# Performance work log

Hardware: AMD Instinct MI355X
Metric: run time of the kernel (lower is better)

Reference implementation:

```python
import jax, jax.numpy as jnp
import numpy as np

NEG_INF = -9e15
ALPHA = 0.2  # LeakyReLU negative slope

N = 8192
D_IN = 512
D_OUT = 256


def setup_inputs() -> dict:
    key = jax.random.key(0)
    k1, k2, k3, k4, k5 = jax.random.split(key, 5)
    features = jax.random.normal(k1, (N, D_IN), dtype=jnp.float32)
    adjacency_matrix = jax.random.randint(k2, (N, N), 0, 2, dtype=jnp.int32)
    # learned params (torch Linear stores [out, in]; we use [in, out] layout)
    s_phi = 1.0 / np.sqrt(D_IN)
    W_phi = jax.random.uniform(k3, (D_IN, D_OUT), jnp.float32, -s_phi, s_phi)
    s_v = 1.0 / np.sqrt(D_OUT)
    w_mu = jax.random.uniform(k4, (D_OUT,), jnp.float32, -s_v, s_v)
    w_xi = jax.random.uniform(k5, (D_OUT,), jnp.float32, -s_v, s_v)
    return {"features": features, "adjacency_matrix": adjacency_matrix,
            "W_phi": W_phi, "w_mu": w_mu, "w_xi": w_xi}


def reference(features, adjacency_matrix, W_phi, w_mu, w_xi):
    h = features @ W_phi                                   # [N, d_out]
    mu = h @ w_mu                                          # [N]
    xi = h @ w_xi                                          # [N]
    e = mu[:, None] + xi[None, :]                          # [N, N] additive scores
    e = jnp.where(e >= 0, e, ALPHA * e)                    # LeakyReLU
    e = jnp.where(adjacency_matrix > 0, e, NEG_INF)        # mask non-edges
    a = jax.nn.softmax(e, axis=1)                          # row softmax (dropout p=0)
    out = a @ h                                            # weighted aggregation
    return jax.nn.elu(out)
```

## Files before the change

kernel.cpp:

```cpp
#include <hip/hip_runtime.h>
#include <cstdint>
#include <cstddef>


#define NN 8192
#define DIN 512
#define DOUT 256

typedef __attribute__((ext_vector_type(8))) short short8;
typedef __attribute__((ext_vector_type(4))) float floatx4;

using uint_as1 = __attribute__((address_space(1))) unsigned int;
using uint_as3 = __attribute__((address_space(3))) unsigned int;

__device__ __forceinline__ void gld_lds16(const void* g, void* l) {
  __builtin_amdgcn_global_load_lds((const uint_as1*)g, (uint_as3*)l, 16, 0, 0);
}

__device__ __forceinline__ unsigned short f2b(float f) {
  unsigned u = __float_as_uint(f);
  u += 0x7fffu + ((u >> 16) & 1u);
  return (unsigned short)(u >> 16);
}
__device__ __forceinline__ float b2f(short s) {
  return __uint_as_float(((unsigned)(unsigned short)s) << 16);
}

__global__ void k_cvt_features(const float* __restrict__ f, unsigned short* __restrict__ fb) {
  int tid = blockIdx.x * 256 + threadIdx.x;
  float4 v = ((const float4*)f)[tid];
  ushort4 o = {f2b(v.x), f2b(v.y), f2b(v.z), f2b(v.w)};
  *(ushort4*)&fb[tid * 4] = o;
}

__global__ void k_prep_wt(const float* __restrict__ w, unsigned short* __restrict__ wt) {
  int tid = blockIdx.x * 256 + threadIdx.x;
  int n = tid >> 9, k = tid & 511;
  wt[n * 512 + k] = f2b(w[k * 256 + n]);
}

__global__ void k_prep_p(const float* __restrict__ w, const float* __restrict__ wmu,
                         const float* __restrict__ wxi, float* __restrict__ pmu,
                         float* __restrict__ pxi) {
  int tid = blockIdx.x * 256 + threadIdx.x;
  int k = tid >> 2, seg = tid & 3;
  float sm = 0.f, sx = 0.f;
  int base = k * 256 + seg * 64;
#pragma unroll
  for (int c = 0; c < 64; c += 4) {
    float4 wv = *(const float4*)&w[base + c];
    float4 mv = *(const float4*)&wmu[seg * 64 + c];
    float4 xv = *(const float4*)&wxi[seg * 64 + c];
    sm += wv.x * mv.x + wv.y * mv.y + wv.z * mv.z + wv.w * mv.w;
    sx += wv.x * xv.x + wv.y * xv.y + wv.z * xv.z + wv.w * xv.w;
  }
  sm += __shfl_xor(sm, 1); sm += __shfl_xor(sm, 2);
  sx += __shfl_xor(sx, 1); sx += __shfl_xor(sx, 2);
  if (seg == 0) { pmu[k] = sm; pxi[k] = sx; }
}

__global__ void k_mu_xi(const unsigned short* __restrict__ fb, const float* __restrict__ pmu,
                        const float* __restrict__ pxi, float* __restrict__ mu,
                        float* __restrict__ xi) {
  int w = threadIdx.x >> 6, l = threadIdx.x & 63;
  int i = blockIdx.x * 4 + w;
  short8 fv = *(const short8*)&fb[i * 512 + l * 8];
  float m = 0.f, x = 0.f;
#pragma unroll
  for (int c = 0; c < 8; ++c) {
    float fvf = b2f(fv[c]);
    m = fmaf(fvf, pmu[l * 8 + c], m);
    x = fmaf(fvf, pxi[l * 8 + c], x);
  }
#pragma unroll
  for (int off = 32; off > 0; off >>= 1) {
    m += __shfl_xor(m, off);
    x += __shfl_xor(x, off);
  }
  if (l == 0) { mu[i] = m; xi[i] = x; }
}

__global__ __launch_bounds__(256, 2) void k_gemm1(const unsigned short* __restrict__ fb,
                                                  const unsigned short* __restrict__ wt,
                                                  unsigned short* __restrict__ ht) {
  __shared__ __align__(16) unsigned short As[64 * 64];
  __shared__ __align__(16) unsigned short Bs[128 * 64];
  int t = threadIdx.x, w = t >> 6, l = t & 63;
  int bm = blockIdx.x >> 1, bn = blockIdx.x & 1;
  int m0 = bm * 64, n0 = bn * 128;
  int lr = l >> 3, lg = l & 7, g = lg ^ lr;
  int kg = l >> 4, ln = l & 15;
  floatx4 zero = {0.f, 0.f, 0.f, 0.f};
  floatx4 acc[4][2];
#pragma unroll
  for (int mf = 0; mf < 4; ++mf)
#pragma unroll
    for (int nf = 0; nf < 2; ++nf) acc[mf][nf] = zero;

  for (int it = 0; it < 8; ++it) {
    int k0 = it * 64;
#pragma unroll
    for (int q = 0; q < 2; ++q) {
      int row = w * 16 + q * 8 + lr;
      const void* gp = fb + (size_t)(m0 + row) * 512 + k0 + g * 8;
      int lb = __builtin_amdgcn_readfirstlane((w * 16 + q * 8) * 64);
      gld_lds16(gp, &As[lb]);
    }
#pragma unroll
    for (int q = 0; q < 4; ++q) {
      int row = w * 32 + q * 8 + lr;
      const void* gp = wt + (size_t)(n0 + row) * 512 + k0 + g * 8;
      int lb = __builtin_amdgcn_readfirstlane((w * 32 + q * 8) * 64);
      gld_lds16(gp, &Bs[lb]);
    }
    __syncthreads();
#pragma unroll
    for (int ks = 0; ks < 2; ++ks) {
      int gg = ks * 4 + kg;
      int swz = (gg ^ (ln & 7)) * 8;
      short8 bfr[2];
#pragma unroll
      for (int nf = 0; nf < 2; ++nf)
        bfr[nf] = *(const short8*)&Bs[(w * 32 + nf * 16 + ln) * 64 + swz];
#pragma unroll
      for (int mf = 0; mf < 4; ++mf) {
        short8 afr = *(const short8*)&As[(mf * 16 + ln) * 64 + swz];
#pragma unroll
        for (int nf = 0; nf < 2; ++nf)
          acc[mf][nf] = __builtin_amdgcn_mfma_f32_16x16x32_bf16(afr, bfr[nf], acc[mf][nf], 0, 0, 0);
      }
    }
    __syncthreads();
  }
#pragma unroll
  for (int mf = 0; mf < 4; ++mf)
#pragma unroll
    for (int nf = 0; nf < 2; ++nf) {
      int ng = n0 + w * 32 + nf * 16 + ln;
      int mg = m0 + mf * 16 + kg * 4;
      ushort4 o = {f2b(acc[mf][nf][0]), f2b(acc[mf][nf][1]),
                   f2b(acc[mf][nf][2]), f2b(acc[mf][nf][3])};
      *(ushort4*)&ht[(size_t)ng * 8192 + mg] = o;
    }
}

__global__ __launch_bounds__(256, 2) void k_attn(const int* __restrict__ adj,
                                                 const unsigned short* __restrict__ ht,
                                                 const float* __restrict__ mu,
                                                 const float* __restrict__ xi,
                                                 float* __restrict__ out) {
  __shared__ __align__(16) unsigned short Bt[256 * 64];
  __shared__ __align__(16) unsigned short Wl[16 * 72];
  __shared__ __align__(16) float xis[8192];
  __shared__ float zinv[16];

  int t = threadIdx.x, w = t >> 6, l = t & 63;
  int i0 = blockIdx.x * 16;
  int rowi = t >> 4, col4 = (t & 15) * 4;
  int lr = l >> 3, lg = l & 7, g = lg ^ lr;
  int kg = l >> 4, ln = l & 15;

  float mu_t = mu[i0 + rowi];
#pragma unroll
  for (int c = 0; c < 8; ++c) {
    int idx = c * 1024 + t * 4;
    *(float4*)&xis[idx] = *(const float4*)&xi[idx];
  }
  floatx4 zero = {0.f, 0.f, 0.f, 0.f};
  floatx4 acc[4];
#pragma unroll
  for (int nf = 0; nf < 4; ++nf) acc[nf] = zero;
  float zsum = 0.f;
  const int* adjrow = adj + (size_t)(i0 + rowi) * 8192 + col4;
  __syncthreads();

  for (int it = 0; it < 128; ++it) {
    int j0 = it * 64;
    int4 a4 = *(const int4*)(adjrow + j0);
    float4 xv = *(const float4*)&xis[j0 + col4];
    float s0 = mu_t + xv.x, s1 = mu_t + xv.y, s2 = mu_t + xv.z, s3 = mu_t + xv.w;
    s0 = fmaxf(s0, 0.2f * s0); s1 = fmaxf(s1, 0.2f * s1);
    s2 = fmaxf(s2, 0.2f * s2); s3 = fmaxf(s3, 0.2f * s3);
    float e0 = __builtin_amdgcn_exp2f(s0 * 1.44269504f);
    float e1 = __builtin_amdgcn_exp2f(s1 * 1.44269504f);
    float e2 = __builtin_amdgcn_exp2f(s2 * 1.44269504f);
    float e3 = __builtin_amdgcn_exp2f(s3 * 1.44269504f);
    float w0 = (a4.x != 0) ? e0 : 0.f;
    float w1 = (a4.y != 0) ? e1 : 0.f;
    float w2 = (a4.z != 0) ? e2 : 0.f;
    float w3 = (a4.w != 0) ? e3 : 0.f;
    zsum += (w0 + w1) + (w2 + w3);
    ushort4 wp = {f2b(w0), f2b(w1), f2b(w2), f2b(w3)};
    *(ushort4*)&Wl[rowi * 72 + col4] = wp;
#pragma unroll
    for (int q = 0; q < 8; ++q) {
      int n = w * 64 + q * 8 + lr;
      const void* gp = ht + (size_t)n * 8192 + j0 + g * 8;
      int lb = __builtin_amdgcn_readfirstlane((w * 64 + q * 8) * 64);
      gld_lds16(gp, &Bt[lb]);
    }
    __syncthreads();
#pragma unroll
    for (int ks = 0; ks < 2; ++ks) {
      int gg = ks * 4 + kg;
      short8 afr = *(const short8*)&Wl[ln * 72 + gg * 8];
#pragma unroll
      for (int nf = 0; nf < 4; ++nf) {
        int n = w * 64 + nf * 16 + ln;
        short8 bfr = *(const short8*)&Bt[n * 64 + ((gg ^ (ln & 7)) * 8)];
        acc[nf] = __builtin_amdgcn_mfma_f32_16x16x32_bf16(afr, bfr, acc[nf], 0, 0, 0);
      }
    }
    __syncthreads();
  }

  float* zb = xis;
  zb[t] = zsum;
  __syncthreads();
  if (t < 16) {
    float s = 0.f;
#pragma unroll
    for (int q = 0; q < 16; ++q) s += zb[t * 16 + q];
    zinv[t] = 1.0f / s;
  }
  __syncthreads();

#pragma unroll
  for (int nf = 0; nf < 4; ++nf) {
    int col = w * 64 + nf * 16 + ln;
#pragma unroll
    for (int r = 0; r < 4; ++r) {
      int row = kg * 4 + r;
      float v = acc[nf][r] * zinv[row];
      v = (v > 0.f) ? v : (__builtin_amdgcn_exp2f(v * 1.44269504f) - 1.f);
      out[(size_t)(i0 + row) * 256 + col] = v;
    }
  }
}

extern "C" void kernel_launch(void* const* d_in, const int* in_sizes, int n_in,
                              void* d_out, int out_size, void* d_ws, size_t ws_size,
                              hipStream_t stream) {
  const float* features = (const float*)d_in[0];
  const int* adjm = (const int*)d_in[1];
  const float* W_phi = (const float*)d_in[2];
  const float* w_mu = (const float*)d_in[3];
  const float* w_xi = (const float*)d_in[4];
  float* out = (float*)d_out;

  char* ws = (char*)d_ws;
  unsigned short* fb  = (unsigned short*)(ws + 0);
  unsigned short* ht  = (unsigned short*)(ws + 8388608);
  unsigned short* wt  = (unsigned short*)(ws + 12582912);
  float* pmu = (float*)(ws + 12845056);
  float* pxi = (float*)(ws + 12847104);
  float* muv = (float*)(ws + 12849152);
  float* xiv = (float*)(ws + 12881920);

  k_cvt_features<<<4096, 256, 0, stream>>>(features, fb);
  k_prep_wt<<<512, 256, 0, stream>>>(W_phi, wt);
  k_prep_p<<<8, 256, 0, stream>>>(W_phi, w_mu, w_xi, pmu, pxi);
  k_mu_xi<<<2048, 256, 0, stream>>>(fb, pmu, pxi, muv, xiv);
  k_gemm1<<<256, 256, 0, stream>>>(fb, wt, ht);
  k_attn<<<512, 256, 0, stream>>>(adjm, ht, muv, xiv, out);
}
```

Before: 505.9 us.

## Split attention aggregation across column chunks with atomic partial sums

The attention kernel now gives each block 64 rows and a quarter of the columns (split-K). The B operand (ht) is read straight from global memory into registers instead of being staged through LDS, and adjacency loads are prefetched one iteration ahead. Partial numerators and softmax denominators are accumulated with float atomics into a zeroed workspace, and a separate final kernel normalizes and applies ELU. This removes the per-iteration barriers and the LDS staging, and each block reads ht once for 64 rows instead of 16. The cost is the atomic traffic, two extra launches, and summation order that is no longer deterministic. It also holds 16 accumulator tiles per thread, which raises register pressure.

```diff
diff --git a/kernel.cpp b/kernel.cpp
--- a/kernel.cpp
+++ b/kernel.cpp
@@ -144,98 +144,119 @@
     }
 }
 
-__global__ __launch_bounds__(256, 2) void k_attn(const int* __restrict__ adj,
-                                                 const unsigned short* __restrict__ ht,
-                                                 const float* __restrict__ mu,
-                                                 const float* __restrict__ xi,
-                                                 float* __restrict__ out) {
-  __shared__ __align__(16) unsigned short Bt[256 * 64];
-  __shared__ __align__(16) unsigned short Wl[16 * 72];
-  __shared__ __align__(16) float xis[8192];
-  __shared__ float zinv[16];
-
+__global__ void k_zero(float* __restrict__ num, float* __restrict__ zbuf) {
+  int b = blockIdx.x, t = threadIdx.x;
+  if (b < 2048) {
+    float4 z4 = {0.f, 0.f, 0.f, 0.f};
+    *(float4*)&num[(b * 256 + t) * 4] = z4;
+  } else {
+    zbuf[(b - 2048) * 256 + t] = 0.f;
+  }
+}
+
+__global__ __launch_bounds__(256, 2) void k_attn3(const int* __restrict__ adj,
+                                                  const unsigned short* __restrict__ ht,
+                                                  const float* __restrict__ mu,
+                                                  const float* __restrict__ xi,
+                                                  float* __restrict__ num,
+                                                  float* __restrict__ zbuf) {
+  __shared__ __align__(16) float xic[2048];
   int t = threadIdx.x, w = t >> 6, l = t & 63;
-  int i0 = blockIdx.x * 16;
-  int rowi = t >> 4, col4 = (t & 15) * 4;
-  int lr = l >> 3, lg = l & 7, g = lg ^ lr;
-  int kg = l >> 4, ln = l & 15;
-
-  float mu_t = mu[i0 + rowi];
-#pragma unroll
-  for (int c = 0; c < 8; ++c) {
-    int idx = c * 1024 + t * 4;
-    *(float4*)&xis[idx] = *(const float4*)&xi[idx];
-  }
+  int ln = l & 15, kg = l >> 4;
+  int bi = blockIdx.x >> 2, bj = blockIdx.x & 3;
+  int i0 = bi * 64, jbase = bj * 2048;
+
+#pragma unroll
+  for (int c = 0; c < 2; ++c) {
+    int idx = t * 8 + c * 4;
+    float4 v = *(const float4*)&xi[jbase + idx];
+    v.x *= 1.44269504f; v.y *= 1.44269504f; v.z *= 1.44269504f; v.w *= 1.44269504f;
+    *(float4*)&xic[idx] = v;
+  }
+  int irow = i0 + w * 16 + ln;
+  float mu_c = mu[irow] * 1.44269504f;
+  __syncthreads();
+
   floatx4 zero = {0.f, 0.f, 0.f, 0.f};
-  floatx4 acc[4];
-#pragma unroll
-  for (int nf = 0; nf < 4; ++nf) acc[nf] = zero;
+  floatx4 acc[16];
+#pragma unroll
+  for (int nf = 0; nf < 16; ++nf) acc[nf] = zero;
+
+  const int4* ap = (const int4*)(adj + (size_t)irow * 8192 + jbase) + kg * 2;
+  int4 a0 = ap[0], a1 = ap[1], b0 = ap[8], b1 = ap[9];
+  const unsigned short* hrow = ht + (size_t)ln * 8192 + jbase + kg * 8;
   float zsum = 0.f;
-  const int* adjrow = adj + (size_t)(i0 + rowi) * 8192 + col4;
-  __syncthreads();
-
-  for (int it = 0; it < 128; ++it) {
-    int j0 = it * 64;
-    int4 a4 = *(const int4*)(adjrow + j0);
-    float4 xv = *(const float4*)&xis[j0 + col4];
-    float s0 = mu_t + xv.x, s1 = mu_t + xv.y, s2 = mu_t + xv.z, s3 = mu_t + xv.w;
-    s0 = fmaxf(s0, 0.2f * s0); s1 = fmaxf(s1, 0.2f * s1);
-    s2 = fmaxf(s2, 0.2f * s2); s3 = fmaxf(s3, 0.2f * s3);
-    float e0 = __builtin_amdgcn_exp2f(s0 * 1.44269504f);
-    float e1 = __builtin_amdgcn_exp2f(s1 * 1.44269504f);
-    float e2 = __builtin_amdgcn_exp2f(s2 * 1.44269504f);
-    float e3 = __builtin_amdgcn_exp2f(s3 * 1.44269504f);
-    float w0 = (a4.x != 0) ? e0 : 0.f;
-    float w1 = (a4.y != 0) ? e1 : 0.f;
-    float w2 = (a4.z != 0) ? e2 : 0.f;
-    float w3 = (a4.w != 0) ? e3 : 0.f;
-    zsum += (w0 + w1) + (w2 + w3);
-    ushort4 wp = {f2b(w0), f2b(w1), f2b(w2), f2b(w3)};
-    *(ushort4*)&Wl[rowi * 72 + col4] = wp;
-#pragma unroll
-    for (int q = 0; q < 8; ++q) {
-      int n = w * 64 + q * 8 + lr;
-      const void* gp = ht + (size_t)n * 8192 + j0 + g * 8;
-      int lb = __builtin_amdgcn_readfirstlane((w * 64 + q * 8) * 64);
-      gld_lds16(gp, &Bt[lb]);
-    }
-    __syncthreads();
-#pragma unroll
-    for (int ks = 0; ks < 2; ++ks) {
-      int gg = ks * 4 + kg;
-      short8 afr = *(const short8*)&Wl[ln * 72 + gg * 8];
-#pragma unroll
-      for (int nf = 0; nf < 4; ++nf) {
-        int n = w * 64 + nf * 16 + ln;
-        short8 bfr = *(const short8*)&Bt[n * 64 + ((gg ^ (ln & 7)) * 8)];
-        acc[nf] = __builtin_amdgcn_mfma_f32_16x16x32_bf16(afr, bfr, acc[nf], 0, 0, 0);
-      }
-    }
-    __syncthreads();
-  }
-
-  float* zb = xis;
-  zb[t] = zsum;
-  __syncthreads();
-  if (t < 16) {
-    float s = 0.f;
-#pragma unroll
-    for (int q = 0; q < 16; ++q) s += zb[t * 16 + q];
-    zinv[t] = 1.0f / s;
-  }
-  __syncthreads();
-
-#pragma unroll
-  for (int nf = 0; nf < 4; ++nf) {
-    int col = w * 64 + nf * 16 + ln;
+
+  for (int it = 0; it < 32; ++it) {
+    int jo = it * 64;
+    int xb = jo + kg * 8;
+    float4 x0  = *(const float4*)&xic[xb];
+    float4 x0b = *(const float4*)&xic[xb + 4];
+    float4 x1  = *(const float4*)&xic[xb + 32];
+    float4 x1b = *(const float4*)&xic[xb + 36];
+
+    int am[16] = {a0.x, a0.y, a0.z, a0.w, a1.x, a1.y, a1.z, a1.w,
+                  b0.x, b0.y, b0.z, b0.w, b1.x, b1.y, b1.z, b1.w};
+    float xv[16] = {x0.x, x0.y, x0.z, x0.w, x0b.x, x0b.y, x0b.z, x0b.w,
+                    x1.x, x1.y, x1.z, x1.w, x1b.x, x1b.y, x1b.z, x1b.w};
+
+    int noff = (it < 31) ? (it + 1) * 16 : 0;
+    a0 = ap[noff]; a1 = ap[noff + 1]; b0 = ap[noff + 8]; b1 = ap[noff + 9];
+
+    float wv[16];
+#pragma unroll
+    for (int c = 0; c < 16; ++c) {
+      float s = mu_c + xv[c];
+      s = fmaxf(s, 0.2f * s);
+      float e = __builtin_amdgcn_exp2f(s);
+      wv[c] = (am[c] != 0) ? e : 0.f;
+      zsum += wv[c];
+    }
+    short8 afr0, afr1;
+#pragma unroll
+    for (int c = 0; c < 8; ++c) {
+      afr0[c] = (short)f2b(wv[c]);
+      afr1[c] = (short)f2b(wv[8 + c]);
+    }
+
+    const unsigned short* hp = hrow + jo;
+#pragma unroll
+    for (int nf = 0; nf < 16; ++nf) {
+      const unsigned short* hn = hp + (size_t)nf * (16 * 8192);
+      short8 bf0 = *(const short8*)hn;
+      short8 bf1 = *(const short8*)(hn + 32);
+      acc[nf] = __builtin_amdgcn_mfma_f32_16x16x32_bf16(afr0, bf0, acc[nf], 0, 0, 0);
+      acc[nf] = __builtin_amdgcn_mfma_f32_16x16x32_bf16(afr1, bf1, acc[nf], 0, 0, 0);
+    }
+  }
+
+  zsum += __shfl_xor(zsum, 16);
+  zsum += __shfl_xor(zsum, 32);
+  if (kg == 0) atomicAdd(&zbuf[irow], zsum);
+
+#pragma unroll
+  for (int nf = 0; nf < 16; ++nf) {
+    int col = nf * 16 + ln;
 #pragma unroll
     for (int r = 0; r < 4; ++r) {
-      int row = kg * 4 + r;
-      float v = acc[nf][r] * zinv[row];
-      v = (v > 0.f) ? v : (__builtin_amdgcn_exp2f(v * 1.44269504f) - 1.f);
-      out[(size_t)(i0 + row) * 256 + col] = v;
-    }
-  }
+      int row = i0 + w * 16 + kg * 4 + r;
+      atomicAdd(&num[(size_t)row * 256 + col], acc[nf][r]);
+    }
+  }
+}
+
+__global__ void k_final(const float* __restrict__ num, const float* __restrict__ zbuf,
+                        float* __restrict__ out) {
+  int tid = blockIdx.x * 256 + threadIdx.x;
+  int i = tid >> 6;
+  float zi = 1.0f / zbuf[i];
+  float4 v = *(const float4*)&num[tid * 4];
+  v.x *= zi; v.y *= zi; v.z *= zi; v.w *= zi;
+  v.x = (v.x > 0.f) ? v.x : (__builtin_amdgcn_exp2f(v.x * 1.44269504f) - 1.f);
+  v.y = (v.y > 0.f) ? v.y : (__builtin_amdgcn_exp2f(v.y * 1.44269504f) - 1.f);
+  v.z = (v.z > 0.f) ? v.z : (__builtin_amdgcn_exp2f(v.z * 1.44269504f) - 1.f);
+  v.w = (v.w > 0.f) ? v.w : (__builtin_amdgcn_exp2f(v.w * 1.44269504f) - 1.f);
+  *(float4*)&out[tid * 4] = v;
 }
 
 extern "C" void kernel_launch(void* const* d_in, const int* in_sizes, int n_in,
@@ -256,11 +277,15 @@
   float* pxi = (float*)(ws + 12847104);
   float* muv = (float*)(ws + 12849152);
   float* xiv = (float*)(ws + 12881920);
+  float* num  = (float*)(ws + 0);
+  float* zbuf = (float*)(ws + 12582912);
 
   k_cvt_features<<<4096, 256, 0, stream>>>(features, fb);
   k_prep_wt<<<512, 256, 0, stream>>>(W_phi, wt);
   k_prep_p<<<8, 256, 0, stream>>>(W_phi, w_mu, w_xi, pmu, pxi);
   k_mu_xi<<<2048, 256, 0, stream>>>(fb, pmu, pxi, muv, xiv);
   k_gemm1<<<256, 256, 0, stream>>>(fb, wt, ht);
-  k_attn<<<512, 256, 0, stream>>>(adjm, ht, muv, xiv, out);
-}
+  k_zero<<<2080, 256, 0, stream>>>(num, zbuf);
+  k_attn3<<<512, 256, 0, stream>>>(adjm, ht, muv, xiv, num, zbuf);
+  k_final<<<2048, 256, 0, stream>>>(num, zbuf, out);
+}
```

Result: slower. 609.7 us (+20.5%).
